# Optimization experiments

Measured on AMD Instinct MI355X. Metric: run time of the kernel, lower is better.

Reference implementation:

```python
import jax, jax.numpy as jnp
import numpy as np

N_CLUSTERS = 256
EMBED_DIM = 128
ALPHA = 1.0


def setup_inputs() -> dict:
    key = jax.random.key(0)
    k1, k2 = jax.random.split(key)
    inputs = jax.random.normal(k1, (200000, EMBED_DIM), dtype=jnp.float32)
    clusters = jax.random.normal(k2, (N_CLUSTERS, EMBED_DIM), dtype=jnp.float32)
    return {"inputs": inputs, "clusters": clusters}


def reference(inputs, clusters):
    # Squared euclidean distance via the GEMM trick instead of an [N, K, D]
    x_sq = jnp.sum(inputs * inputs, axis=1, keepdims=True)          # [N, 1]
    c_sq = jnp.sum(clusters * clusters, axis=1)[None, :]             # [1, K]
    cross = inputs @ clusters.T                                      # [N, K]
    dist2 = jnp.maximum(x_sq + c_sq - 2.0 * cross, 0.0)              # [N, K]
    q = 1.0 / (1.0 + dist2 / ALPHA)
    q = q ** ((ALPHA + 1.0) / 2.0)
    q = q / jnp.sum(q, axis=1, keepdims=True)
    return q
```

## Files before the change

### kernel.cpp

```cpp
#include <hip/hip_runtime.h>


#define DIM 128
#define NK  256

typedef __attribute__((ext_vector_type(8))) short short8;
typedef __attribute__((ext_vector_type(4))) float floatx4;

__device__ __forceinline__ unsigned short bf16_rne(float f) {
    unsigned int u = __float_as_uint(f);
    return (unsigned short)((u + 0x7fffu + ((u >> 16) & 1u)) >> 16);
}
__device__ __forceinline__ float bf16_f(unsigned short h) {
    return __uint_as_float(((unsigned int)h) << 16);
}

__global__ void prep_clusters(const float* __restrict__ c,
                              unsigned short* __restrict__ wb,
                              float* __restrict__ wcsq)
{
    if (blockIdx.x < 8) {
        const int gid  = blockIdx.x * 512 + threadIdx.x;
        const int lane = gid & 63;
        const int ks   = (gid >> 6) & 3;
        const int ct   = gid >> 8;
        const int lm   = lane & 15;
        const int q4   = lane >> 4;
        const int col  = ct * 16 + lm;
        const float4* cg = (const float4*)(c + col * DIM + ks * 32 + q4 * 8);
        float4 v0 = cg[0], v1 = cg[1];
        const float* f0 = (const float*)&v0;
        const float* f1 = (const float*)&v1;
        union { unsigned short u[8]; short8 v; } B;
        #pragma unroll
        for (int i = 0; i < 4; ++i) B.u[i] = bf16_rne(f0[i]);
        #pragma unroll
        for (int i = 0; i < 4; ++i) B.u[4 + i] = bf16_rne(f1[i]);
        ((short8*)wb)[gid] = B.v;
    } else {
        const int t = threadIdx.x;
        const int col = t >> 1, half = t & 1;
        const float4* cg = (const float4*)(c + col * DIM + half * 64);
        float s = 0.f;
        #pragma unroll
        for (int i = 0; i < 16; ++i) {
            float4 v = cg[i];
            s = fmaf(v.x, v.x, s); s = fmaf(v.y, v.y, s);
            s = fmaf(v.z, v.z, s); s = fmaf(v.w, v.w, s);
        }
        s += __shfl_xor(s, 1);
        if (!half) wcsq[col] = s;
    }
}

__device__ __forceinline__ void prefetch_x(const float* __restrict__ x,
                                           int t, int wave, int lm, int q4,
                                           float4 pf[8]) {
    const float* xr = x + ((size_t)t * 64 + wave * 16 + lm) * DIM;
    #pragma unroll
    for (int ks = 0; ks < 4; ++ks) {
        const float4* xg = (const float4*)(xr + ks * 32 + q4 * 8);
        pf[2 * ks]     = xg[0];
        pf[2 * ks + 1] = xg[1];
    }
}

__global__ __launch_bounds__(256, 1) void cluster_q_v5(
    const float* __restrict__ x,
    const unsigned short* __restrict__ wb,
    const float* __restrict__ wcsq,
    float* __restrict__ out,
    const int NT)
{
    __shared__ __align__(16) unsigned short bs[32768];
    __shared__ float csq_s[NK];
    __shared__ __align__(16) float lt[4][2][4][264];

    const int tid  = threadIdx.x;
    const int wave = tid >> 6;
    const int lane = tid & 63;
    const int lm   = lane & 15;
    const int q4   = lane >> 4;

    csq_s[tid] = wcsq[tid];
    for (int i = tid; i < 4096; i += 256) {
        float4 v = ((const float4*)wb)[i];
        *(float4*)&bs[i * 8] = v;
    }
    __syncthreads();

    float4 pf[8];
    int t = blockIdx.x;
    if (t < NT) prefetch_x(x, t, wave, lm, q4, pf);

    while (t < NT) {
        short8 ah[4], al[4];
        float xq = 0.f;
        #pragma unroll
        for (int ks = 0; ks < 4; ++ks) {
            const float* f0 = (const float*)&pf[2 * ks];
            const float* f1 = (const float*)&pf[2 * ks + 1];
            union { unsigned short u[8]; short8 v; } H, L;
            #pragma unroll
            for (int i = 0; i < 4; ++i) {
                float f = f0[i];
                xq = fmaf(f, f, xq);
                unsigned short h = bf16_rne(f);
                H.u[i] = h;
                L.u[i] = bf16_rne(f - bf16_f(h));
            }
            #pragma unroll
            for (int i = 0; i < 4; ++i) {
                float f = f1[i];
                xq = fmaf(f, f, xq);
                unsigned short h = bf16_rne(f);
                H.u[4 + i] = h;
                L.u[4 + i] = bf16_rne(f - bf16_f(h));
            }
            ah[ks] = H.v;
            al[ks] = L.v;
        }
        xq += __shfl_xor(xq, 16);
        xq += __shfl_xor(xq, 32);

        floatx4 acc[16];
        #pragma unroll
        for (int ct = 0; ct < 16; ++ct) {
            floatx4 a = (floatx4){0.f, 0.f, 0.f, 0.f};
            #pragma unroll
            for (int ks = 0; ks < 4; ++ks) {
                short8 b = *(const short8*)&bs[(ct * 256 + ks * 64 + lane) * 8];
                a = __builtin_amdgcn_mfma_f32_16x16x32_bf16(ah[ks], b, a, 0, 0, 0);
                a = __builtin_amdgcn_mfma_f32_16x16x32_bf16(al[ks], b, a, 0, 0, 0);
            }
            acc[ct] = a;
        }

        const int tn = t + (int)gridDim.x;
        if (tn < NT) prefetch_x(x, tn, wave, lm, q4, pf);

        float xs4[4];
        #pragma unroll
        for (int r = 0; r < 4; ++r) xs4[r] = __shfl(xq, q4 * 4 + r);

        float rsum[4] = {0.f, 0.f, 0.f, 0.f};
        #pragma unroll
        for (int ct = 0; ct < 16; ++ct) {
            const float cq = csq_s[ct * 16 + lm];
            #pragma unroll
            for (int r = 0; r < 4; ++r) {
                float d2 = fmaf(-2.f, acc[ct][r], xs4[r] + cq);
                d2 = fmaxf(d2, 0.f);
                float q = __builtin_amdgcn_rcpf(1.f + d2);
                acc[ct][r] = q;
                rsum[r] += q;
            }
        }
        #pragma unroll
        for (int r = 0; r < 4; ++r) {
            rsum[r] += __shfl_xor(rsum[r], 1);
            rsum[r] += __shfl_xor(rsum[r], 2);
            rsum[r] += __shfl_xor(rsum[r], 4);
            rsum[r] += __shfl_xor(rsum[r], 8);
            rsum[r] = __builtin_amdgcn_rcpf(rsum[r]);
        }

        __builtin_amdgcn_sched_barrier(0);

        #pragma unroll
        for (int r = 0; r < 4; ++r) {
            float* lw = &lt[wave][r & 1][q4][0];
            const float inv = rsum[r];
            #pragma unroll
            for (int ct = 0; ct < 16; ++ct)
                lw[ct * 16 + lm] = acc[ct][r] * inv;
            asm volatile("s_waitcnt lgkmcnt(0)" ::: "memory");
            #pragma unroll
            for (int j = 0; j < 4; ++j) {
                const floatx4 v = *(const floatx4*)&lt[wave][r & 1][j][lane * 4];
                __builtin_nontemporal_store(v,
                    (floatx4*)(out + ((size_t)t * 64 + wave * 16 + j * 4 + r) * NK + lane * 4));
            }
        }

        t = tn;
    }
}

extern "C" void kernel_launch(void* const* d_in, const int* in_sizes, int n_in,
                              void* d_out, int out_size, void* d_ws, size_t ws_size,
                              hipStream_t stream) {
    const float* x = (const float*)d_in[0];
    const float* c = (const float*)d_in[1];
    float* out = (float*)d_out;
    unsigned short* wb = (unsigned short*)d_ws;
    float* wcsq = (float*)((char*)d_ws + 65536);
    const int N = in_sizes[0] / DIM;
    const int NT = N / 64;

    prep_clusters<<<dim3(9), dim3(512), 0, stream>>>(c, wb, wcsq);
    const int grid = NT < 512 ? NT : 512;
    cluster_q_v5<<<dim3(grid), dim3(256), 0, stream>>>(x, wb, wcsq, out, NT);
}
```

Before: 289.9 us.

## Widen blocks to eight waves with two blocks per CU and per-wave 16-row strips

Blocks grow from 4 to 8 waves and launch bounds change to 512 threads with 2 blocks per CU. Each wave now owns an independent 16-row strip indexed by s, so a partial final block is handled by masking inactive waves. The goal is more resident waves per CU to hide global-load and store latency while the cluster matrix is shared in LDS across more waves. In exchange, the register budget per thread shrinks, which risks spilling the 16 accumulator vectors and prefetch buffers, and LDS use per block roughly doubles for the staging area.

```diff
diff --git a/kernel.cpp b/kernel.cpp
--- a/kernel.cpp
+++ b/kernel.cpp
@@ -54,9 +54,9 @@
 }
 
 __device__ __forceinline__ void prefetch_x(const float* __restrict__ x,
-                                           int t, int wave, int lm, int q4,
+                                           int s, int lm, int q4,
                                            float4 pf[8]) {
-    const float* xr = x + ((size_t)t * 64 + wave * 16 + lm) * DIM;
+    const float* xr = x + ((size_t)s * 16 + lm) * DIM;
     #pragma unroll
     for (int ks = 0; ks < 4; ++ks) {
         const float4* xg = (const float4*)(xr + ks * 32 + q4 * 8);
@@ -65,16 +65,17 @@
     }
 }
 
-__global__ __launch_bounds__(256, 1) void cluster_q_v5(
+__global__ __launch_bounds__(512, 2) void cluster_q_v6(
     const float* __restrict__ x,
     const unsigned short* __restrict__ wb,
     const float* __restrict__ wcsq,
     float* __restrict__ out,
-    const int NT)
+    const int S,
+    const int NTB)
 {
     __shared__ __align__(16) unsigned short bs[32768];
     __shared__ float csq_s[NK];
-    __shared__ __align__(16) float lt[4][2][4][264];
+    __shared__ __align__(16) float lt[8][2][4][264];
 
     const int tid  = threadIdx.x;
     const int wave = tid >> 6;
@@ -82,8 +83,8 @@
     const int lm   = lane & 15;
     const int q4   = lane >> 4;
 
-    csq_s[tid] = wcsq[tid];
-    for (int i = tid; i < 4096; i += 256) {
+    if (tid < NK) csq_s[tid] = wcsq[tid];
+    for (int i = tid; i < 4096; i += 512) {
         float4 v = ((const float4*)wb)[i];
         *(float4*)&bs[i * 8] = v;
     }
@@ -91,99 +92,108 @@
 
     float4 pf[8];
     int t = blockIdx.x;
-    if (t < NT) prefetch_x(x, t, wave, lm, q4, pf);
-
-    while (t < NT) {
+    int s = t * 8 + wave;
+    if (t < NTB && s < S) prefetch_x(x, s, lm, q4, pf);
+
+    while (t < NTB) {
+        const bool active = (s < S);
         short8 ah[4], al[4];
         float xq = 0.f;
-        #pragma unroll
-        for (int ks = 0; ks < 4; ++ks) {
-            const float* f0 = (const float*)&pf[2 * ks];
-            const float* f1 = (const float*)&pf[2 * ks + 1];
-            union { unsigned short u[8]; short8 v; } H, L;
-            #pragma unroll
-            for (int i = 0; i < 4; ++i) {
-                float f = f0[i];
-                xq = fmaf(f, f, xq);
-                unsigned short h = bf16_rne(f);
-                H.u[i] = h;
-                L.u[i] = bf16_rne(f - bf16_f(h));
-            }
-            #pragma unroll
-            for (int i = 0; i < 4; ++i) {
-                float f = f1[i];
-                xq = fmaf(f, f, xq);
-                unsigned short h = bf16_rne(f);
-                H.u[4 + i] = h;
-                L.u[4 + i] = bf16_rne(f - bf16_f(h));
-            }
-            ah[ks] = H.v;
-            al[ks] = L.v;
+        floatx4 acc[16];
+
+        if (active) {
+            #pragma unroll
+            for (int ks = 0; ks < 4; ++ks) {
+                const float* f0 = (const float*)&pf[2 * ks];
+                const float* f1 = (const float*)&pf[2 * ks + 1];
+                union { unsigned short u[8]; short8 v; } H, L;
+                #pragma unroll
+                for (int i = 0; i < 4; ++i) {
+                    float f = f0[i];
+                    xq = fmaf(f, f, xq);
+                    unsigned short h = bf16_rne(f);
+                    H.u[i] = h;
+                    L.u[i] = bf16_rne(f - bf16_f(h));
+                }
+                #pragma unroll
+                for (int i = 0; i < 4; ++i) {
+                    float f = f1[i];
+                    xq = fmaf(f, f, xq);
+                    unsigned short h = bf16_rne(f);
+                    H.u[4 + i] = h;
+                    L.u[4 + i] = bf16_rne(f - bf16_f(h));
+                }
+                ah[ks] = H.v;
+                al[ks] = L.v;
+            }
+            xq += __shfl_xor(xq, 16);
+            xq += __shfl_xor(xq, 32);
+
+            #pragma unroll
+            for (int ct = 0; ct < 16; ++ct) {
+                floatx4 a = (floatx4){0.f, 0.f, 0.f, 0.f};
+                #pragma unroll
+                for (int ks = 0; ks < 4; ++ks) {
+                    short8 b = *(const short8*)&bs[(ct * 256 + ks * 64 + lane) * 8];
+                    a = __builtin_amdgcn_mfma_f32_16x16x32_bf16(ah[ks], b, a, 0, 0, 0);
+                    a = __builtin_amdgcn_mfma_f32_16x16x32_bf16(al[ks], b, a, 0, 0, 0);
+                }
+                acc[ct] = a;
+            }
         }
-        xq += __shfl_xor(xq, 16);
-        xq += __shfl_xor(xq, 32);
-
-        floatx4 acc[16];
-        #pragma unroll
-        for (int ct = 0; ct < 16; ++ct) {
-            floatx4 a = (floatx4){0.f, 0.f, 0.f, 0.f};
-            #pragma unroll
-            for (int ks = 0; ks < 4; ++ks) {
-                short8 b = *(const short8*)&bs[(ct * 256 + ks * 64 + lane) * 8];
-                a = __builtin_amdgcn_mfma_f32_16x16x32_bf16(ah[ks], b, a, 0, 0, 0);
-                a = __builtin_amdgcn_mfma_f32_16x16x32_bf16(al[ks], b, a, 0, 0, 0);
-            }
-            acc[ct] = a;
+
+        const int tn = t + (int)gridDim.x;
+        const int sn = tn * 8 + wave;
+        if (tn < NTB && sn < S) prefetch_x(x, sn, lm, q4, pf);
+
+        if (active) {
+            float xs4[4];
+            #pragma unroll
+            for (int r = 0; r < 4; ++r) xs4[r] = __shfl(xq, q4 * 4 + r);
+
+            float rsum[4] = {0.f, 0.f, 0.f, 0.f};
+            #pragma unroll
+            for (int ct = 0; ct < 16; ++ct) {
+                const float cq = csq_s[ct * 16 + lm];
+                #pragma unroll
+                for (int r = 0; r < 4; ++r) {
+                    float d2 = fmaf(-2.f, acc[ct][r], xs4[r] + cq);
+                    d2 = fmaxf(d2, 0.f);
+                    float q = __builtin_amdgcn_rcpf(1.f + d2);
+                    acc[ct][r] = q;
+                    rsum[r] += q;
+                }
+            }
+            #pragma unroll
+            for (int r = 0; r < 4; ++r) {
+                rsum[r] += __shfl_xor(rsum[r], 1);
+                rsum[r] += __shfl_xor(rsum[r], 2);
+                rsum[r] += __shfl_xor(rsum[r], 4);
+                rsum[r] += __shfl_xor(rsum[r], 8);
+                rsum[r] = __builtin_amdgcn_rcpf(rsum[r]);
+            }
+
+            __builtin_amdgcn_sched_barrier(0);
+
+            #pragma unroll
+            for (int r = 0; r < 4; ++r) {
+                float* lw = &lt[wave][r & 1][q4][0];
+                const float inv = rsum[r];
+                #pragma unroll
+                for (int ct = 0; ct < 16; ++ct)
+                    lw[ct * 16 + lm] = acc[ct][r] * inv;
+                asm volatile("s_waitcnt lgkmcnt(0)" ::: "memory");
+                #pragma unroll
+                for (int j = 0; j < 4; ++j) {
+                    const floatx4 v = *(const floatx4*)&lt[wave][r & 1][j][lane * 4];
+                    __builtin_nontemporal_store(v,
+                        (floatx4*)(out + ((size_t)s * 16 + j * 4 + r) * NK + lane * 4));
+                }
+            }
         }
 
-        const int tn = t + (int)gridDim.x;
-        if (tn < NT) prefetch_x(x, tn, wave, lm, q4, pf);
-
-        float xs4[4];
-        #pragma unroll
-        for (int r = 0; r < 4; ++r) xs4[r] = __shfl(xq, q4 * 4 + r);
-
-        float rsum[4] = {0.f, 0.f, 0.f, 0.f};
-        #pragma unroll
-        for (int ct = 0; ct < 16; ++ct) {
-            const float cq = csq_s[ct * 16 + lm];
-            #pragma unroll
-            for (int r = 0; r < 4; ++r) {
-                float d2 = fmaf(-2.f, acc[ct][r], xs4[r] + cq);
-                d2 = fmaxf(d2, 0.f);
-                float q = __builtin_amdgcn_rcpf(1.f + d2);
-                acc[ct][r] = q;
-                rsum[r] += q;
-            }
-        }
-        #pragma unroll
-        for (int r = 0; r < 4; ++r) {
-            rsum[r] += __shfl_xor(rsum[r], 1);
-            rsum[r] += __shfl_xor(rsum[r], 2);
-            rsum[r] += __shfl_xor(rsum[r], 4);
-            rsum[r] += __shfl_xor(rsum[r], 8);
-            rsum[r] = __builtin_amdgcn_rcpf(rsum[r]);
-        }
-
-        __builtin_amdgcn_sched_barrier(0);
-
-        #pragma unroll
-        for (int r = 0; r < 4; ++r) {
-            float* lw = &lt[wave][r & 1][q4][0];
-            const float inv = rsum[r];
-            #pragma unroll
-            for (int ct = 0; ct < 16; ++ct)
-                lw[ct * 16 + lm] = acc[ct][r] * inv;
-            asm volatile("s_waitcnt lgkmcnt(0)" ::: "memory");
-            #pragma unroll
-            for (int j = 0; j < 4; ++j) {
-                const floatx4 v = *(const floatx4*)&lt[wave][r & 1][j][lane * 4];
-                __builtin_nontemporal_store(v,
-                    (floatx4*)(out + ((size_t)t * 64 + wave * 16 + j * 4 + r) * NK + lane * 4));
-            }
-        }
-
         t = tn;
+        s = sn;
     }
 }
 
@@ -196,9 +206,10 @@
     unsigned short* wb = (unsigned short*)d_ws;
     float* wcsq = (float*)((char*)d_ws + 65536);
     const int N = in_sizes[0] / DIM;
-    const int NT = N / 64;
+    const int S = N / 16;
+    const int NTB = (S + 7) / 8;
 
     prep_clusters<<<dim3(9), dim3(512), 0, stream>>>(c, wb, wcsq);
-    const int grid = NT < 512 ? NT : 512;
-    cluster_q_v5<<<dim3(grid), dim3(256), 0, stream>>>(x, wb, wcsq, out, NT);
-}
+    const int grid = NTB < 512 ? NTB : 512;
+    cluster_q_v6<<<dim3(grid), dim3(512), 0, stream>>>(x, wb, wcsq, out, S, NTB);
+}
```

Measured after the change: 291.1 us. No clear change (+0.4%).
